# Kernel tuning notes

Measured on AMD Instinct MI355X. Metric: run time of the kernel, lower is better.

The kernel has to match this reference:

```python
import jax, jax.numpy as jnp
import numpy as np

B, C, H, W = 2, 64, 96, 96
DQK = C // 8  # query/key channel dim = 8


def setup_inputs() -> dict:
    key = jax.random.key(0)
    ks = jax.random.split(key, 8)
    s = 0.05
    x = jax.random.normal(ks[0], (B, C, H, W), dtype=jnp.float32)
    Wq = jax.random.normal(ks[1], (DQK, C), dtype=jnp.float32) * s
    bq = jax.random.normal(ks[2], (DQK,), dtype=jnp.float32) * s
    Wk = jax.random.normal(ks[3], (DQK, C), dtype=jnp.float32) * s
    bk = jax.random.normal(ks[4], (DQK,), dtype=jnp.float32) * s
    Wv = jax.random.normal(ks[5], (C, C), dtype=jnp.float32) * s
    bv = jax.random.normal(ks[6], (C,), dtype=jnp.float32) * s
    gamma = jax.random.normal(ks[7], (1,), dtype=jnp.float32) * s
    return {"x": x, "Wq": Wq, "bq": bq, "Wk": Wk, "bk": bk,
            "Wv": Wv, "bv": bv, "gamma": gamma}


def _attend(x, Wq, bq, Wk, bk, Wv, bv, gamma):
    b, c, h, w = x.shape
    p = h * w
    xf = x.reshape(b, c, p)                                    # [B,C,P]
    # 1x1 convs == per-pixel linear maps
    q = jnp.einsum('dc,bcp->bpd', Wq, xf) + bq                 # [B,P,d]
    k = jnp.einsum('dc,bcp->bdp', Wk, xf) + bk[None, :, None]  # [B,d,P]
    v = jnp.einsum('oc,bcp->bop', Wv, xf) + bv[None, :, None]  # [B,C,P]
    # energy[b,i,j] = q_i . k_j ; softmax over keys j (no 1/sqrt(d) scale,
    # matching the original module)
    energy = jnp.einsum('bpd,bdq->bpq', q, k)                  # [B,P,P]
    attn = jax.nn.softmax(energy, axis=-1)                     # [B,P,P]
    out = jnp.einsum('bcq,bpq->bcp', v, attn)                  # [B,C,P]
    out = out.reshape(b, c, h, w)
    return gamma * out + x


def reference(x, Wq, bq, Wk, bk, Wv, bv, gamma):
    return _attend(x, Wq, bq, Wk, bk, Wv, bv, gamma)
```

## Files before the change

kernel.cpp:

```cpp
#include <hip/hip_runtime.h>
#include <hip/hip_bf16.h>
#include <stdint.h>

#define BB 2
#define CC 64
#define PP 9216
#define QTILES 144
#define LOG2E 1.4426950408889634f
#define SCH_BC 12599160.0f

typedef unsigned short ushort;
typedef __attribute__((ext_vector_type(8))) short short8;
typedef __attribute__((ext_vector_type(4))) float floatx4;
typedef __attribute__((ext_vector_type(4))) int intx4;

__device__ __forceinline__ ushort f2bf(float f) {
    unsigned int u = __float_as_uint(f);
    u = (u + 0x7fffu + ((u >> 16) & 1u)) >> 16;
    return (ushort)u;
}

__device__ __forceinline__ unsigned int exp2_pk_bf16(float e0, float e1) {
    const float t0 = fmaf(e0, 128.f, SCH_BC);
    const float t1 = fmaf(e1, 128.f, SCH_BC);
    return __builtin_amdgcn_perm(__float_as_uint(t1), __float_as_uint(t0),
                                 0x05040100u);
}

__device__ __forceinline__ void gload16_lds(const void* g, void* lds_base) {
    __builtin_amdgcn_global_load_lds(
        (const __attribute__((address_space(1))) unsigned int*)g,
        (__attribute__((address_space(3))) unsigned int*)lds_base, 16, 0, 0);
}

__global__ __launch_bounds__(256)
void proj6(const float* __restrict__ x,
           const float* __restrict__ Wq, const float* __restrict__ bq,
           const float* __restrict__ Wk, const float* __restrict__ bk,
           const float* __restrict__ Wv, const float* __restrict__ bv,
           ushort* __restrict__ qbuf, ushort* __restrict__ kbuf,
           ushort* __restrict__ vfw)
{
    const int tid = threadIdx.x;
    const int px  = tid & 63;
    const int og  = __builtin_amdgcn_readfirstlane(tid >> 6);
    const int blk = blockIdx.x;
    const int b     = blk / (4 * QTILES);
    const int rem   = blk % (4 * QTILES);
    const int ptile = rem >> 2;
    const int rq    = rem & 3;
    const int p     = ptile * 64 + px;
    const int r0    = rq * 20 + og * 5;

    const float* wr[5];
#pragma unroll
    for (int r = 0; r < 5; ++r) {
        const int row = r0 + r;
        wr[r] = (row < 8) ? (Wq + row * 64)
              : (row < 16) ? (Wk + (row - 8) * 64)
              : (Wv + (row - 16) * 64);
    }

    const float* xb = x + (size_t)b * 64 * PP + p;
    float acc[5] = {0.f, 0.f, 0.f, 0.f, 0.f};

#pragma unroll 1
    for (int c0 = 0; c0 < 64; c0 += 16) {
        float xv[16];
#pragma unroll
        for (int i = 0; i < 16; ++i)
            xv[i] = xb[(size_t)(c0 + i) * PP];
#pragma unroll
        for (int i = 0; i < 16; ++i) {
#pragma unroll
            for (int r = 0; r < 5; ++r)
                acc[r] = fmaf(wr[r][c0 + i], xv[i], acc[r]);
        }
    }

#pragma unroll
    for (int r = 0; r < 5; ++r) {
        const int row = r0 + r;
        if (row < 8) {
            const float v = (acc[r] + bq[row]) * LOG2E;
            qbuf[((size_t)b * PP + p) * 8 + row] = f2bf(v);
        } else if (row < 16) {
            const float v = acc[r] + bk[row - 8];
            kbuf[((size_t)b * PP + p) * 8 + (row - 8)] = f2bf(v);
        } else {
            const int co = row - 16;
            const float v = acc[r] + bv[co];
            const int pl = p & 31;
            const int ps = (p & ~31) | ((((pl >> 2) & 3) << 3) | (((pl >> 4) & 1) << 2) | (pl & 3));
            vfw[((size_t)b * 64 + co) * PP + ps] = f2bf(v);
        }
    }
}

__global__ __launch_bounds__(128, 3)
void attn13(const ushort* __restrict__ qbuf, const ushort* __restrict__ kbuf,
            const ushort* __restrict__ vfw,
            ushort* __restrict__ accp, float* __restrict__ lsump,
            int keysPerG, int numTiles)
{
    __shared__ __align__(16) char sbuf[27904];
    float* smerge = (float*)sbuf;
    float* slsum  = (float*)(sbuf + 27648);

    const int tid  = threadIdx.x;
    const int lane = tid & 63;
    const int kh   = tid >> 6;
    const int col  = lane & 15;
    const int quad = lane >> 4;

    const int qt = blockIdx.x >> 3;
    const int gb = blockIdx.x & 7;
    const int b  = gb % BB;
    const int g  = gb / BB;
    const int q0 = qt * 64;

    const short8 zf = {0, 0, 0, 0, 0, 0, 0, 0};
    const short vone = (short)0x3F80;
    const short8 vones = {vone, vone, vone, vone, vone, vone, vone, vone};

    short8 qfragB[4];
#pragma unroll
    for (int qh = 0; qh < 4; ++qh)
        qfragB[qh] = (quad == 0)
            ? *(const short8*)(qbuf + ((size_t)b * PP + q0 + qh * 16 + col) * 8)
            : zf;

    floatx4 acc[4][4];
#pragma unroll
    for (int qh = 0; qh < 4; ++qh)
#pragma unroll
        for (int cb = 0; cb < 4; ++cb) acc[qh][cb] = (floatx4){0.f, 0.f, 0.f, 0.f};
    floatx4 accLh[4];
#pragma unroll
    for (int qh = 0; qh < 4; ++qh) accLh[qh] = (floatx4){0.f, 0.f, 0.f, 0.f};

    const ushort* kB = kbuf + (size_t)b * PP * 8;
    const ushort* vB = vfw + (size_t)b * 64 * PP;
    const int kwbase = g * keysPerG;

    const int vr = lane >> 3;
    const int vc = (lane & 7) ^ vr;

    auto stage = [&](int t) {
        const int kw = kwbase + t * 64;
        char* Vb = sbuf + 9216 * (t % 3);
        gload16_lds(kB + (size_t)(kw + lane) * 8, Vb + 8192);
        const int j0 = kh * 4;
#pragma unroll
        for (int j = 0; j < 4; ++j) {
            const int r = (j0 + j) * 8 + vr;
            gload16_lds(vB + (size_t)r * PP + kw + vc * 8, Vb + (j0 + j) * 1024);
        }
    };

    auto compute = [&](int t) {
        const char* Vb = sbuf + 9216 * (t % 3);
        const ushort* Kl = (const ushort*)(Vb + 8192);
        const short8 kf0 = *(const short8*)(Kl + (kh * 32 + col) * 8);
        const short8 kf1 = *(const short8*)(Kl + (kh * 32 + 16 + col) * 8);
        short8 vf[4];
        const int ce = (kh * 4 + quad) ^ (col & 7);
#pragma unroll
        for (int cb = 0; cb < 4; ++cb)
            vf[cb] = *(const short8*)(Vb + ((cb * 16 + col) * 8 + ce) * 16);

#pragma unroll
        for (int qh = 0; qh < 4; ++qh) {
            const floatx4 E0 = __builtin_amdgcn_mfma_f32_16x16x32_bf16(
                kf0, qfragB[qh], (floatx4){0.f, 0.f, 0.f, 0.f}, 0, 0, 0);
            const floatx4 E1 = __builtin_amdgcn_mfma_f32_16x16x32_bf16(
                kf1, qfragB[qh], (floatx4){0.f, 0.f, 0.f, 0.f}, 0, 0, 0);

            intx4 pi;
            pi.x = (int)exp2_pk_bf16(E0[0], E0[1]);
            pi.y = (int)exp2_pk_bf16(E0[2], E0[3]);
            pi.z = (int)exp2_pk_bf16(E1[0], E1[1]);
            pi.w = (int)exp2_pk_bf16(E1[2], E1[3]);
            const short8 pf = __builtin_bit_cast(short8, pi);

            accLh[qh] = __builtin_amdgcn_mfma_f32_16x16x32_bf16(vones, pf, accLh[qh], 0, 0, 0);
#pragma unroll
            for (int cb = 0; cb < 4; ++cb)
                acc[qh][cb] = __builtin_amdgcn_mfma_f32_16x16x32_bf16(
                    vf[cb], pf, acc[qh][cb], 0, 0, 0);
        }
    };

    stage(0);
    stage(1);
    for (int t = 0; t < numTiles - 1; ++t) {
        asm volatile("s_waitcnt vmcnt(5)" ::: "memory");
        __builtin_amdgcn_s_barrier();
        __builtin_amdgcn_sched_barrier(0);
        if (t + 2 < numTiles) stage(t + 2);
        compute(t);
    }
    asm volatile("s_waitcnt vmcnt(0)" ::: "memory");
    __builtin_amdgcn_s_barrier();
    __builtin_amdgcn_sched_barrier(0);
    compute(numTiles - 1);
    __syncthreads();

    if (kh == 1) {
#pragma unroll
        for (int qh = 0; qh < 4; ++qh)
#pragma unroll
            for (int cb = 0; cb < 4; ++cb)
#pragma unroll
                for (int r = 0; r < 4; ++r)
                    smerge[(cb * 16 + quad * 4 + r) * 64 + qh * 16 + col] = acc[qh][cb][r];
        if (quad == 0)
#pragma unroll
            for (int qh = 0; qh < 4; ++qh)
                slsum[qh * 16 + col] = accLh[qh][0];
    }
    __syncthreads();
    if (kh == 0) {
        ushort* ab = accp + ((size_t)g * BB + b) * CC * PP;
#pragma unroll
        for (int qh = 0; qh < 4; ++qh)
#pragma unroll
            for (int cb = 0; cb < 4; ++cb)
#pragma unroll
                for (int r = 0; r < 4; ++r) {
                    const int c = cb * 16 + quad * 4 + r;
                    const float v = acc[qh][cb][r] + smerge[c * 64 + qh * 16 + col];
                    ab[(size_t)c * PP + q0 + qh * 16 + col] = f2bf(v);
                }
        if (quad == 0) {
            float* lb = lsump + ((size_t)g * BB + b) * PP + q0;
#pragma unroll
            for (int qh = 0; qh < 4; ++qh)
                lb[qh * 16 + col] = accLh[qh][0] + slsum[qh * 16 + col];
        }
    }
}

__global__ __launch_bounds__(256)
void combine(const ushort* __restrict__ accp, const float* __restrict__ lsump,
             const float* __restrict__ x, const float* __restrict__ gamma,
             float* __restrict__ out, int G)
{
    const size_t i8 = ((size_t)blockIdx.x * 256 + threadIdx.x) * 8;
    const int b = (int)(i8 / ((size_t)CC * PP));
    const int p = (int)(i8 % PP);
    const float gm = gamma[0];

    float asum[8] = {}, lst[8] = {};
    for (int g = 0; g < G; ++g) {
        const uint4 av = *(const uint4*)(accp + (size_t)g * (BB * CC * PP) + i8);
        const unsigned int u[4] = {av.x, av.y, av.z, av.w};
#pragma unroll
        for (int k = 0; k < 4; ++k) {
            asum[2 * k]     += __uint_as_float(u[k] << 16);
            asum[2 * k + 1] += __uint_as_float(u[k] & 0xffff0000u);
        }
        const float* lp = lsump + ((size_t)g * BB + b) * PP + p;
        const float4 l0 = *(const float4*)lp;
        const float4 l1 = *(const float4*)(lp + 4);
        lst[0] += l0.x; lst[1] += l0.y; lst[2] += l0.z; lst[3] += l0.w;
        lst[4] += l1.x; lst[5] += l1.y; lst[6] += l1.z; lst[7] += l1.w;
    }

    const float4 x0 = *(const float4*)(x + i8);
    const float4 x1 = *(const float4*)(x + i8 + 4);
    float o[8] = {x0.x, x0.y, x0.z, x0.w, x1.x, x1.y, x1.z, x1.w};
#pragma unroll
    for (int j = 0; j < 8; ++j)
        o[j] = fmaf(asum[j], gm / fmaxf(lst[j], 1e-30f), o[j]);
    *(float4*)(out + i8)     = make_float4(o[0], o[1], o[2], o[3]);
    *(float4*)(out + i8 + 4) = make_float4(o[4], o[5], o[6], o[7]);
}

extern "C" void kernel_launch(void* const* d_in, const int* in_sizes, int n_in,
                              void* d_out, int out_size, void* d_ws, size_t ws_size,
                              hipStream_t stream)
{
    const float* x     = (const float*)d_in[0];
    const float* Wq    = (const float*)d_in[1];
    const float* bq    = (const float*)d_in[2];
    const float* Wk    = (const float*)d_in[3];
    const float* bk    = (const float*)d_in[4];
    const float* Wv    = (const float*)d_in[5];
    const float* bv    = (const float*)d_in[6];
    const float* gamma = (const float*)d_in[7];
    float* out = (float*)d_out;

    const size_t nQK  = (size_t)BB * PP * 8;
    const size_t nV   = (size_t)BB * CC * PP;
    const int G = 4;
    const int keysPerG = PP / G;
    const int numTiles = keysPerG / 64;

    ushort* qbuf = (ushort*)d_ws;
    ushort* kbuf = qbuf + nQK;
    ushort* vfw  = kbuf + nQK;
    ushort* accp = vfw + nV;
    float* lsump = (float*)(accp + (size_t)G * nV);
    (void)ws_size;

    proj6<<<dim3(BB * 4 * QTILES), dim3(256), 0, stream>>>(
        x, Wq, bq, Wk, bk, Wv, bv, qbuf, kbuf, vfw);
    attn13<<<dim3(QTILES * 8), dim3(128), 0, stream>>>(
        qbuf, kbuf, vfw, accp, lsump, keysPerG, numTiles);
    combine<<<dim3(576), dim3(256), 0, stream>>>(
        accp, lsump, x, gamma, out, G);
}
```

Before: 118.2 us.

## Split attention block query tile across four waves to halve per-wave accumulators

```diff
diff --git a/kernel.cpp b/kernel.cpp
--- a/kernel.cpp
+++ b/kernel.cpp
@@ -97,8 +97,8 @@
     }
 }
 
-__global__ __launch_bounds__(128, 3)
-void attn13(const ushort* __restrict__ qbuf, const ushort* __restrict__ kbuf,
+__global__ __launch_bounds__(256, 4)
+void attn14(const ushort* __restrict__ qbuf, const ushort* __restrict__ kbuf,
             const ushort* __restrict__ vfw,
             ushort* __restrict__ accp, float* __restrict__ lsump,
             int keysPerG, int numTiles)
@@ -109,7 +109,9 @@
 
     const int tid  = threadIdx.x;
     const int lane = tid & 63;
-    const int kh   = tid >> 6;
+    const int wid  = tid >> 6;
+    const int kh   = wid & 1;
+    const int qh2  = wid >> 1;
     const int col  = lane & 15;
     const int quad = lane >> 4;
 
@@ -117,27 +119,27 @@
     const int gb = blockIdx.x & 7;
     const int b  = gb % BB;
     const int g  = gb / BB;
-    const int q0 = qt * 64;
+    const int q0 = qt * 64 + qh2 * 32;
 
     const short8 zf = {0, 0, 0, 0, 0, 0, 0, 0};
     const short vone = (short)0x3F80;
     const short8 vones = {vone, vone, vone, vone, vone, vone, vone, vone};
 
-    short8 qfragB[4];
-#pragma unroll
-    for (int qh = 0; qh < 4; ++qh)
-        qfragB[qh] = (quad == 0)
-            ? *(const short8*)(qbuf + ((size_t)b * PP + q0 + qh * 16 + col) * 8)
+    short8 qfragB[2];
+#pragma unroll
+    for (int qhl = 0; qhl < 2; ++qhl)
+        qfragB[qhl] = (quad == 0)
+            ? *(const short8*)(qbuf + ((size_t)b * PP + q0 + qhl * 16 + col) * 8)
             : zf;
 
-    floatx4 acc[4][4];
-#pragma unroll
-    for (int qh = 0; qh < 4; ++qh)
-#pragma unroll
-        for (int cb = 0; cb < 4; ++cb) acc[qh][cb] = (floatx4){0.f, 0.f, 0.f, 0.f};
-    floatx4 accLh[4];
-#pragma unroll
-    for (int qh = 0; qh < 4; ++qh) accLh[qh] = (floatx4){0.f, 0.f, 0.f, 0.f};
+    floatx4 acc[2][4];
+#pragma unroll
+    for (int qhl = 0; qhl < 2; ++qhl)
+#pragma unroll
+        for (int cb = 0; cb < 4; ++cb) acc[qhl][cb] = (floatx4){0.f, 0.f, 0.f, 0.f};
+    floatx4 accLh[2];
+#pragma unroll
+    for (int qhl = 0; qhl < 2; ++qhl) accLh[qhl] = (floatx4){0.f, 0.f, 0.f, 0.f};
 
     const ushort* kB = kbuf + (size_t)b * PP * 8;
     const ushort* vB = vfw + (size_t)b * 64 * PP;
@@ -150,11 +152,11 @@
         const int kw = kwbase + t * 64;
         char* Vb = sbuf + 9216 * (t % 3);
         gload16_lds(kB + (size_t)(kw + lane) * 8, Vb + 8192);
-        const int j0 = kh * 4;
-#pragma unroll
-        for (int j = 0; j < 4; ++j) {
-            const int r = (j0 + j) * 8 + vr;
-            gload16_lds(vB + (size_t)r * PP + kw + vc * 8, Vb + (j0 + j) * 1024);
+#pragma unroll
+        for (int j = 0; j < 2; ++j) {
+            const int jj = wid * 2 + j;
+            const int r  = jj * 8 + vr;
+            gload16_lds(vB + (size_t)r * PP + kw + vc * 8, Vb + jj * 1024);
         }
     };
 
@@ -170,11 +172,11 @@
             vf[cb] = *(const short8*)(Vb + ((cb * 16 + col) * 8 + ce) * 16);
 
 #pragma unroll
-        for (int qh = 0; qh < 4; ++qh) {
+        for (int qhl = 0; qhl < 2; ++qhl) {
             const floatx4 E0 = __builtin_amdgcn_mfma_f32_16x16x32_bf16(
-                kf0, qfragB[qh], (floatx4){0.f, 0.f, 0.f, 0.f}, 0, 0, 0);
+                kf0, qfragB[qhl], (floatx4){0.f, 0.f, 0.f, 0.f}, 0, 0, 0);
             const floatx4 E1 = __builtin_amdgcn_mfma_f32_16x16x32_bf16(
-                kf1, qfragB[qh], (floatx4){0.f, 0.f, 0.f, 0.f}, 0, 0, 0);
+                kf1, qfragB[qhl], (floatx4){0.f, 0.f, 0.f, 0.f}, 0, 0, 0);
 
             intx4 pi;
             pi.x = (int)exp2_pk_bf16(E0[0], E0[1]);
@@ -183,18 +185,18 @@
             pi.w = (int)exp2_pk_bf16(E1[2], E1[3]);
             const short8 pf = __builtin_bit_cast(short8, pi);
 
-            accLh[qh] = __builtin_amdgcn_mfma_f32_16x16x32_bf16(vones, pf, accLh[qh], 0, 0, 0);
+            accLh[qhl] = __builtin_amdgcn_mfma_f32_16x16x32_bf16(vones, pf, accLh[qhl], 0, 0, 0);
 #pragma unroll
             for (int cb = 0; cb < 4; ++cb)
-                acc[qh][cb] = __builtin_amdgcn_mfma_f32_16x16x32_bf16(
-                    vf[cb], pf, acc[qh][cb], 0, 0, 0);
+                acc[qhl][cb] = __builtin_amdgcn_mfma_f32_16x16x32_bf16(
+                    vf[cb], pf, acc[qhl][cb], 0, 0, 0);
         }
     };
 
     stage(0);
     stage(1);
     for (int t = 0; t < numTiles - 1; ++t) {
-        asm volatile("s_waitcnt vmcnt(5)" ::: "memory");
+        asm volatile("s_waitcnt vmcnt(3)" ::: "memory");
         __builtin_amdgcn_s_barrier();
         __builtin_amdgcn_sched_barrier(0);
         if (t + 2 < numTiles) stage(t + 2);
@@ -208,35 +210,38 @@
 
     if (kh == 1) {
 #pragma unroll
-        for (int qh = 0; qh < 4; ++qh)
+        for (int qhl = 0; qhl < 2; ++qhl)
 #pragma unroll
             for (int cb = 0; cb < 4; ++cb)
 #pragma unroll
                 for (int r = 0; r < 4; ++r)
-                    smerge[(cb * 16 + quad * 4 + r) * 64 + qh * 16 + col] = acc[qh][cb][r];
+                    smerge[((size_t)qh2 * 64 + cb * 16 + quad * 4 + r) * 32
+                           + qhl * 16 + col] = acc[qhl][cb][r];
         if (quad == 0)
 #pragma unroll
-            for (int qh = 0; qh < 4; ++qh)
-                slsum[qh * 16 + col] = accLh[qh][0];
+            for (int qhl = 0; qhl < 2; ++qhl)
+                slsum[qh2 * 32 + qhl * 16 + col] = accLh[qhl][0];
     }
     __syncthreads();
     if (kh == 0) {
         ushort* ab = accp + ((size_t)g * BB + b) * CC * PP;
 #pragma unroll
-        for (int qh = 0; qh < 4; ++qh)
+        for (int qhl = 0; qhl < 2; ++qhl)
 #pragma unroll
             for (int cb = 0; cb < 4; ++cb)
 #pragma unroll
                 for (int r = 0; r < 4; ++r) {
                     const int c = cb * 16 + quad * 4 + r;
-                    const float v = acc[qh][cb][r] + smerge[c * 64 + qh * 16 + col];
-                    ab[(size_t)c * PP + q0 + qh * 16 + col] = f2bf(v);
+                    const float v = acc[qhl][cb][r]
+                        + smerge[((size_t)qh2 * 64 + c) * 32 + qhl * 16 + col];
+                    ab[(size_t)c * PP + q0 + qhl * 16 + col] = f2bf(v);
                 }
         if (quad == 0) {
             float* lb = lsump + ((size_t)g * BB + b) * PP + q0;
 #pragma unroll
-            for (int qh = 0; qh < 4; ++qh)
-                lb[qh * 16 + col] = accLh[qh][0] + slsum[qh * 16 + col];
+            for (int qhl = 0; qhl < 2; ++qhl)
+                lb[qhl * 16 + col] = accLh[qhl][0]
+                    + slsum[qh2 * 32 + qhl * 16 + col];
         }
     }
 }
@@ -306,7 +311,7 @@
 
     proj6<<<dim3(BB * 4 * QTILES), dim3(256), 0, stream>>>(
         x, Wq, bq, Wk, bk, Wv, bv, qbuf, kbuf, vfw);
-    attn13<<<dim3(QTILES * 8), dim3(128), 0, stream>>>(
+    attn14<<<dim3(QTILES * 8), dim3(256), 0, stream>>>(
         qbuf, kbuf, vfw, accp, lsump, keysPerG, numTiles);
     combine<<<dim3(576), dim3(256), 0, stream>>>(
         accp, lsump, x, gamma, out, G);
```

New measurement: 119.3 us. No clear change (+1.0%).
